# Performance work log

Measured on AMD Instinct MI355X. Metric: run time of the kernel, lower is better.

The kernel has to match this reference:

```python
import jax, jax.numpy as jnp
import numpy as np

N_NODES = 100000


def sage_layer(h, src, dst, w_self, w_neigh, b):
    """DGL SAGEConv with mean aggregator: fc_self(h) + fc_neigh(mean_in_neigh(h)) + b."""
    msg = h[src]  # [E, d] gather source features
    agg = jax.ops.segment_sum(msg, dst, num_segments=N_NODES)  # [N, d]
    deg = jax.ops.segment_sum(jnp.ones((src.shape[0],), h.dtype), dst, num_segments=N_NODES)
    mean = agg / jnp.maximum(deg, 1.0)[:, None]
    return h @ w_self + mean @ w_neigh + b


def setup_inputs() -> dict:
    key = jax.random.key(0)
    ks = jax.random.split(key, 12)
    N, E = N_NODES, 1600000
    in_f, hid, n_cls = 4, 128, 2

    def glorot(k, shape):
        lim = float(np.sqrt(6.0 / (shape[0] + shape[1])))
        return jax.random.uniform(k, shape, jnp.float32, -lim, lim)

    return {
        "feats": jax.random.normal(ks[0], (N, in_f), jnp.float32),
        "src": jax.random.randint(ks[1], (E,), 0, N),
        "dst": jax.random.randint(ks[2], (E,), 0, N),
        "w_self1": glorot(ks[3], (in_f, hid)),
        "w_neigh1": glorot(ks[4], (in_f, hid)),
        "b1": jnp.zeros((hid,), jnp.float32),
        "w_self2": glorot(ks[5], (hid, hid)),
        "w_neigh2": glorot(ks[6], (hid, hid)),
        "b2": jnp.zeros((hid,), jnp.float32),
        "w_out": glorot(ks[7], (hid, n_cls)),
        "b_out": jnp.zeros((n_cls,), jnp.float32),
    }


def reference(feats, src, dst, w_self1, w_neigh1, b1, w_self2, w_neigh2, b2, w_out, b_out):
    h = jax.nn.relu(sage_layer(feats, src, dst, w_self1, w_neigh1, b1))
    h = jax.nn.relu(sage_layer(h, src, dst, w_self2, w_neigh2, b2))
    return h @ w_out + b_out  # [N, num_classes] logits
```

## Files before the change

kernel.cpp:

```cpp
#include <hip/hip_runtime.h>
#include <hip/hip_bf16.h>

static constexpr int N = 100000;
static constexpr int HID = 128;
static constexpr int NBKT = (N + 127) / 128;
static constexpr int BCAP = 2560;
static constexpr int BEPB = 4096;

typedef short v8s __attribute__((ext_vector_type(8)));
typedef float v4f __attribute__((ext_vector_type(4)));
typedef unsigned short u16x8 __attribute__((ext_vector_type(8)));

static __device__ __forceinline__ unsigned short f2bf(float x) {
  unsigned u = __float_as_uint(x);
  return (unsigned short)((u + 0x7fffu + ((u >> 16) & 1u)) >> 16);
}
static __device__ __forceinline__ float bf2f(unsigned short u) {
  return __uint_as_float(((unsigned)u) << 16);
}

__global__ void k_wprep(const float* __restrict__ ws2, const float* __restrict__ wn2,
                        unsigned short* __restrict__ wp, unsigned* __restrict__ bcur) {
  int id = blockIdx.x * 64 + threadIdx.x;
  if (id < NBKT) bcur[id] = (unsigned)id * BCAP;
  int b = blockIdx.x;
  int mat = b >> 5;
  int ks = (b >> 3) & 3;
  int cf = b & 7;
  int l = threadIdx.x;
  const float* W = mat ? wn2 : ws2;
  int col = cf * 16 + (l & 15);
  int k0 = ks * 32 + (l >> 4) * 8;
  u16x8 h8, l8;
#pragma unroll
  for (int i = 0; i < 8; ++i) {
    float w = W[(k0 + i) * 128 + col];
    unsigned short h = f2bf(w);
    h8[i] = h;
    l8[i] = f2bf(w - bf2f(h));
  }
  int fhi = (ks * 4 + mat) * 8 + cf;
  int flo = (ks * 4 + mat + 2) * 8 + cf;
  *reinterpret_cast<u16x8*>(wp + fhi * 512 + l * 8) = h8;
  *reinterpret_cast<u16x8*>(wp + flo * 512 + l * 8) = l8;
}

__global__ __launch_bounds__(256) void k_bucket(const int* __restrict__ src,
                                                const int* __restrict__ dst,
                                                unsigned* __restrict__ bcur,
                                                unsigned* __restrict__ bucket, int E) {
  __shared__ unsigned hist[NBKT];
  __shared__ unsigned base[NBKT];
  for (int i = threadIdx.x; i < NBKT; i += 256) hist[i] = 0;
  __syncthreads();
  const int e0 = blockIdx.x * BEPB;
  const int n = min(e0 + BEPB, E) - e0;

  unsigned pk[16];
  int bk[16];
#pragma unroll
  for (int i = 0; i < 16; ++i) {
    int e = threadIdx.x + 256 * i;
    if (e < n) {
      int d = __builtin_nontemporal_load(dst + e0 + e);
      int s = __builtin_nontemporal_load(src + e0 + e);
      int b = d >> 7;
      pk[i] = ((unsigned)s << 7) | (unsigned)(d & 127);
      bk[i] = b;
      atomicAdd(&hist[b], 1u);
    } else {
      bk[i] = -1;
      pk[i] = 0;
    }
  }
  __syncthreads();
  for (int i = threadIdx.x; i < NBKT; i += 256) {
    unsigned h = hist[i];
    base[i] = h ? atomicAdd(&bcur[i], h) : 0u;
    hist[i] = 0;
  }
  __syncthreads();
#pragma unroll
  for (int i = 0; i < 16; ++i) {
    if (bk[i] >= 0) {
      unsigned pos = base[bk[i]] + atomicAdd(&hist[bk[i]], 1u);
      bucket[pos] = pk[i];
    }
  }
}

__global__ void k_bucketscan(const unsigned* __restrict__ bcur, unsigned* __restrict__ bbase) {
  __shared__ unsigned s[1024];
  int t = threadIdx.x;
  unsigned v = (t < NBKT) ? (bcur[t] - (unsigned)t * BCAP) : 0u;
  s[t] = v;
  __syncthreads();
  for (int off = 1; off < 1024; off <<= 1) {
    unsigned x = (t >= off) ? s[t - off] : 0u;
    __syncthreads();
    s[t] += x;
    __syncthreads();
  }
  if (t < NBKT) bbase[t] = s[t] - v;
}

__global__ __launch_bounds__(256) void k_csr(const unsigned* __restrict__ bcur,
                                             const unsigned* __restrict__ bbase,
                                             const unsigned* __restrict__ bucket,
                                             unsigned* __restrict__ cnt,
                                             unsigned* __restrict__ roff,
                                             int* __restrict__ csr) {
  const int b = blockIdx.x;
  const unsigned segbase = (unsigned)b * BCAP;
  const unsigned n = bcur[b] - segbase;
  const int v0 = b << 7;
  __shared__ unsigned h[128];
  __shared__ unsigned rowoff[128];
  __shared__ unsigned s[128];
  if (threadIdx.x < 128) h[threadIdx.x] = 0;
  __syncthreads();

  unsigned pk[10];
#pragma unroll
  for (int i = 0; i < 10; ++i) {
    unsigned idx = threadIdx.x + 256u * i;
    if (idx < n) {
      pk[i] = bucket[segbase + idx];
      atomicAdd(&h[pk[i] & 127u], 1u);
    } else {
      pk[i] = 0xffffffffu;
    }
  }
  __syncthreads();

  unsigned val = (threadIdx.x < 128) ? h[threadIdx.x] : 0u;
  if (threadIdx.x < 128) s[threadIdx.x] = val;
  __syncthreads();
  for (int off = 1; off < 128; off <<= 1) {
    unsigned x = (threadIdx.x < 128 && threadIdx.x >= off) ? s[threadIdx.x - off] : 0u;
    __syncthreads();
    if (threadIdx.x < 128) s[threadIdx.x] += x;
    __syncthreads();
  }
  if (threadIdx.x < 128) {
    int v = v0 + threadIdx.x;
    if (v < N) {
      unsigned rstart = bbase[b] + s[threadIdx.x] - val;
      rowoff[threadIdx.x] = rstart;
      roff[v] = rstart;
      cnt[v] = val;
    }
    h[threadIdx.x] = 0;
  }
  __syncthreads();

#pragma unroll
  for (int i = 0; i < 10; ++i) {
    if (pk[i] != 0xffffffffu) {
      unsigned dl = pk[i] & 127u;
      unsigned pos = rowoff[dl] + atomicAdd(&h[dl], 1u);
      csr[pos] = (int)(pk[i] >> 7);
    }
  }
}

__global__ void k_layer1(const float* __restrict__ feats, const unsigned* __restrict__ cnt,
                         const unsigned* __restrict__ roff, const int* __restrict__ csr,
                         const float* __restrict__ ws1, const float* __restrict__ wn1,
                         const float* __restrict__ b1, unsigned short* __restrict__ h1) {
  const int v = blockIdx.x * 16 + (threadIdx.x >> 4);
  const int l = threadIdx.x & 15;
  if (v >= N) return;
  const unsigned c = cnt[v];
  const unsigned start = roff[v];
  float4 acc = make_float4(0.f, 0.f, 0.f, 0.f);
  for (unsigned e = l; e < c; e += 16) {
    int s = csr[start + e];
    float4 f = *reinterpret_cast<const float4*>(feats + 4 * s);
    acc.x += f.x; acc.y += f.y; acc.z += f.z; acc.w += f.w;
  }
#pragma unroll
  for (int off = 1; off < 16; off <<= 1) {
    acc.x += __shfl_xor(acc.x, off);
    acc.y += __shfl_xor(acc.y, off);
    acc.z += __shfl_xor(acc.z, off);
    acc.w += __shfl_xor(acc.w, off);
  }
  float inv = 1.0f / fmaxf((float)c, 1.0f);
  float m0 = acc.x * inv, m1 = acc.y * inv, m2 = acc.z * inv, m3 = acc.w * inv;
  float4 fv = *reinterpret_cast<const float4*>(feats + 4 * v);
  const int c0 = l * 8;
  unsigned o[4];
#pragma unroll
  for (int half = 0; half < 2; ++half) {
    float4 bv = *reinterpret_cast<const float4*>(b1 + c0 + 4 * half);
    float ob[4] = {bv.x, bv.y, bv.z, bv.w};
#pragma unroll
    for (int k = 0; k < 4; ++k) {
      float4 wsv = *reinterpret_cast<const float4*>(ws1 + k * 128 + c0 + 4 * half);
      float4 wnv = *reinterpret_cast<const float4*>(wn1 + k * 128 + c0 + 4 * half);
      float fk = (k == 0) ? fv.x : (k == 1) ? fv.y : (k == 2) ? fv.z : fv.w;
      float mk = (k == 0) ? m0 : (k == 1) ? m1 : (k == 2) ? m2 : m3;
      ob[0] += fk * wsv.x + mk * wnv.x;
      ob[1] += fk * wsv.y + mk * wnv.y;
      ob[2] += fk * wsv.z + mk * wnv.z;
      ob[3] += fk * wsv.w + mk * wnv.w;
    }
#pragma unroll
    for (int jj = 0; jj < 2; ++jj) {
      float lo = fmaxf(ob[2 * jj], 0.f), hi = fmaxf(ob[2 * jj + 1], 0.f);
      o[2 * half + jj] = (unsigned)f2bf(lo) | (((unsigned)f2bf(hi)) << 16);
    }
  }
  *reinterpret_cast<uint4*>(h1 + (size_t)v * HID + c0) =
      make_uint4(o[0], o[1], o[2], o[3]);
}

__global__ void k_agg(const unsigned* __restrict__ cnt, const unsigned* __restrict__ roff,
                      const int* __restrict__ csr, const unsigned short* __restrict__ h1,
                      unsigned short* __restrict__ mean) {
  const int wv = threadIdx.x >> 6;
  const int lane = threadIdx.x & 63;
  const int hl = lane & 31;
  const int v = blockIdx.x * 8 + wv * 2 + (lane >> 5);
  if (v >= N) return;
  const unsigned c = cnt[v];
  const unsigned start = roff[v];
  const unsigned short* __restrict__ hrow = h1 + hl * 4;

  float a0 = 0.f, a1 = 0.f, a2 = 0.f, a3 = 0.f;
  float b0 = 0.f, b1 = 0.f, b2 = 0.f, b3 = 0.f;

  const unsigned cm = c & ~3u;
  unsigned e = 0;
  for (; e < cm; e += 4) {
    int s[4];
#pragma unroll
    for (int q = 0; q < 4; ++q) s[q] = csr[start + e + q];
    uint2 pk[4];
#pragma unroll
    for (int q = 0; q < 4; ++q)
      pk[q] = *reinterpret_cast<const uint2*>(hrow + (size_t)s[q] * HID);
#pragma unroll
    for (int q = 0; q < 4; ++q) {
      float f0 = __uint_as_float(pk[q].x << 16);
      float f1 = __uint_as_float(pk[q].x & 0xffff0000u);
      float f2 = __uint_as_float(pk[q].y << 16);
      float f3 = __uint_as_float(pk[q].y & 0xffff0000u);
      if (q & 1) { b0 += f0; b1 += f1; b2 += f2; b3 += f3; }
      else       { a0 += f0; a1 += f1; a2 += f2; a3 += f3; }
    }
  }
  for (; e < c; ++e) {
    int s = csr[start + e];
    uint2 pk = *reinterpret_cast<const uint2*>(hrow + (size_t)s * HID);
    a0 += __uint_as_float(pk.x << 16);
    a1 += __uint_as_float(pk.x & 0xffff0000u);
    a2 += __uint_as_float(pk.y << 16);
    a3 += __uint_as_float(pk.y & 0xffff0000u);
  }
  float inv = 1.0f / fmaxf((float)c, 1.0f);
  a0 = (a0 + b0) * inv; a1 = (a1 + b1) * inv;
  a2 = (a2 + b2) * inv; a3 = (a3 + b3) * inv;
  uint2 o;
  o.x = (unsigned)f2bf(a0) | (((unsigned)f2bf(a1)) << 16);
  o.y = (unsigned)f2bf(a2) | (((unsigned)f2bf(a3)) << 16);
  *reinterpret_cast<uint2*>(mean + (size_t)v * HID + hl * 4) = o;
}

__global__ __launch_bounds__(256) void k_l2_mfma(
    const unsigned short* __restrict__ h1, const unsigned short* __restrict__ mean,
    const unsigned short* __restrict__ wp, const float* __restrict__ b2,
    const float* __restrict__ wout, const float* __restrict__ bout,
    float* __restrict__ out) {
  const int l = threadIdx.x & 63;
  const int wv = threadIdx.x >> 6;
  const size_t vbase = (size_t)blockIdx.x * 64 + (size_t)wv * 16;
  const int rlane = l & 15;
  const int kg = l >> 4;

  size_t hr = vbase + rlane;
  if (hr >= N) hr = N - 1;
  v8s ah[4], am[4];
#pragma unroll
  for (int ks = 0; ks < 4; ++ks) {
    size_t off = hr * HID + ks * 32 + kg * 8;
    ah[ks] = *reinterpret_cast<const v8s*>(h1 + off);
    am[ks] = *reinterpret_cast<const v8s*>(mean + off);
  }

  v4f acc[8];
#pragma unroll
  for (int cf = 0; cf < 8; ++cf) acc[cf] = (v4f)(0.f);

#pragma unroll
  for (int ks = 0; ks < 4; ++ks) {
#pragma unroll
    for (int m = 0; m < 4; ++m) {
#pragma unroll
      for (int cf = 0; cf < 8; ++cf) {
        v8s bf = *reinterpret_cast<const v8s*>(wp + ((ks * 4 + m) * 8 + cf) * 512 + l * 8);
        acc[cf] = __builtin_amdgcn_mfma_f32_16x16x32_bf16(
            (m & 1) ? am[ks] : ah[ks], bf, acc[cf], 0, 0, 0);
      }
    }
  }

  float b2c[8], w0c[8], w1c[8];
#pragma unroll
  for (int cf = 0; cf < 8; ++cf) {
    int col = cf * 16 + rlane;
    b2c[cf] = b2[col];
    w0c[cf] = wout[col * 2 + 0];
    w1c[cf] = wout[col * 2 + 1];
  }
  const float bo0 = bout[0], bo1 = bout[1];
#pragma unroll
  for (int j = 0; j < 4; ++j) {
    float s0 = 0.f, s1 = 0.f;
#pragma unroll
    for (int cf = 0; cf < 8; ++cf) {
      float h2 = fmaxf(acc[cf][j] + b2c[cf], 0.f);
      s0 += h2 * w0c[cf];
      s1 += h2 * w1c[cf];
    }
#pragma unroll
    for (int off = 1; off < 16; off <<= 1) {
      s0 += __shfl_xor(s0, off);
      s1 += __shfl_xor(s1, off);
    }
    size_t row = vbase + kg * 4 + j;
    if (row < N) {
      if (rlane == 0) out[row * 2 + 0] = s0 + bo0;
      if (rlane == 1) out[row * 2 + 1] = s1 + bo1;
    }
  }
}

extern "C" void kernel_launch(void* const* d_in, const int* in_sizes, int n_in,
                              void* d_out, int out_size, void* d_ws, size_t ws_size,
                              hipStream_t stream) {
  const float* feats = (const float*)d_in[0];
  const int* src = (const int*)d_in[1];
  const int* dst = (const int*)d_in[2];
  const float* ws1 = (const float*)d_in[3];
  const float* wn1 = (const float*)d_in[4];
  const float* b1 = (const float*)d_in[5];
  const float* ws2 = (const float*)d_in[6];
  const float* wn2 = (const float*)d_in[7];
  const float* b2 = (const float*)d_in[8];
  const float* wout = (const float*)d_in[9];
  const float* bout = (const float*)d_in[10];
  float* out = (float*)d_out;
  const int E = in_sizes[1];

  char* p = (char*)d_ws;
  unsigned* bcur = (unsigned*)p;             p += 784 * 4;
  unsigned* bbase = (unsigned*)p;            p += 784 * 4;
  unsigned* bucket = (unsigned*)p;           p += (size_t)NBKT * BCAP * 4;
  int* csr = (int*)p;                        p += (size_t)E * 4;
  unsigned* cnt = (unsigned*)p;              p += (size_t)N * 4;
  unsigned* roff = (unsigned*)p;             p += (size_t)N * 4;
  unsigned short* h1 = (unsigned short*)p;   p += (size_t)N * HID * 2;
  unsigned short* mean = (unsigned short*)p; p += (size_t)N * HID * 2;
  unsigned short* wp = (unsigned short*)p;

  int bgrid = (E + BEPB - 1) / BEPB;
  k_wprep<<<64, 64, 0, stream>>>(ws2, wn2, wp, bcur);
  k_bucket<<<bgrid, 256, 0, stream>>>(src, dst, bcur, bucket, E);
  k_bucketscan<<<1, 1024, 0, stream>>>(bcur, bbase);
  k_csr<<<NBKT, 256, 0, stream>>>(bcur, bbase, bucket, cnt, roff, csr);
  k_layer1<<<(N + 15) / 16, 256, 0, stream>>>(feats, cnt, roff, csr, ws1, wn1, b1, h1);
  k_agg<<<(N + 7) / 8, 256, 0, stream>>>(cnt, roff, csr, h1, mean);
  k_l2_mfma<<<(N + 63) / 64, 256, 0, stream>>>(h1, mean, wp, b2, wout, bout, out);
}
```

Baseline: 168.6 us.

## Locally sort edges by bucket before scatter; double rows per wave in layer-2 MFMA

The bucketing kernel now stages each block's edges in shared memory and counting-sorts them by destination bucket with a block-wide prefix scan. The global writes then go out in bucket-contiguous runs, which makes them more coalesced than the previous random scatter. The layer-2 MFMA kernel now processes two 16-row fragments per wave, so each weight fragment loaded from memory feeds two MFMAs. The cost is a much larger shared-memory footprint and extra scan barriers in k_bucket, plus more registers and half as many blocks in k_l2_mfma.

```diff
diff --git a/kernel.cpp b/kernel.cpp
--- a/kernel.cpp
+++ b/kernel.cpp
@@ -49,43 +49,65 @@
                                                 const int* __restrict__ dst,
                                                 unsigned* __restrict__ bcur,
                                                 unsigned* __restrict__ bucket, int E) {
+  __shared__ unsigned pk_s[BEPB];
+  __shared__ unsigned short bk_s[BEPB];
+  __shared__ unsigned short rk_s[BEPB];
+  __shared__ unsigned sorted_pk[BEPB];
+  __shared__ unsigned short sorted_bk[BEPB];
   __shared__ unsigned hist[NBKT];
-  __shared__ unsigned base[NBKT];
-  for (int i = threadIdx.x; i < NBKT; i += 256) hist[i] = 0;
+  __shared__ unsigned lstart[NBKT];
+  __shared__ unsigned gadj[NBKT];
+  __shared__ unsigned s256[256];
+  __shared__ unsigned carry_s;
+  const int t = threadIdx.x;
+  for (int i = t; i < NBKT; i += 256) hist[i] = 0;
+  if (t == 0) carry_s = 0;
   __syncthreads();
   const int e0 = blockIdx.x * BEPB;
   const int n = min(e0 + BEPB, E) - e0;
 
-  unsigned pk[16];
-  int bk[16];
-#pragma unroll
-  for (int i = 0; i < 16; ++i) {
-    int e = threadIdx.x + 256 * i;
-    if (e < n) {
-      int d = __builtin_nontemporal_load(dst + e0 + e);
-      int s = __builtin_nontemporal_load(src + e0 + e);
-      int b = d >> 7;
-      pk[i] = ((unsigned)s << 7) | (unsigned)(d & 127);
-      bk[i] = b;
-      atomicAdd(&hist[b], 1u);
-    } else {
-      bk[i] = -1;
-      pk[i] = 0;
-    }
-  }
-  __syncthreads();
-  for (int i = threadIdx.x; i < NBKT; i += 256) {
-    unsigned h = hist[i];
-    base[i] = h ? atomicAdd(&bcur[i], h) : 0u;
-    hist[i] = 0;
-  }
-  __syncthreads();
-#pragma unroll
-  for (int i = 0; i < 16; ++i) {
-    if (bk[i] >= 0) {
-      unsigned pos = base[bk[i]] + atomicAdd(&hist[bk[i]], 1u);
-      bucket[pos] = pk[i];
-    }
+  for (int i = t; i < n; i += 256) {
+    int d = __builtin_nontemporal_load(dst + e0 + i);
+    int s = __builtin_nontemporal_load(src + e0 + i);
+    int p = d >> 7;
+    pk_s[i] = ((unsigned)s << 7) | (unsigned)(d & 127);
+    bk_s[i] = (unsigned short)p;
+    rk_s[i] = (unsigned short)atomicAdd(&hist[p], 1u);
+  }
+  __syncthreads();
+
+  for (int base = 0; base < NBKT; base += 256) {
+    int idx = base + t;
+    unsigned v = (idx < NBKT) ? hist[idx] : 0u;
+    s256[t] = v;
+    __syncthreads();
+    for (int off = 1; off < 256; off <<= 1) {
+      unsigned x = (t >= off) ? s256[t - off] : 0u;
+      __syncthreads();
+      s256[t] += x;
+      __syncthreads();
+    }
+    if (idx < NBKT) lstart[idx] = carry_s + s256[t] - v;
+    __syncthreads();
+    if (t == 255) carry_s += s256[255];
+    __syncthreads();
+  }
+
+  for (int i = t; i < NBKT; i += 256) {
+    unsigned c = hist[i];
+    gadj[i] = c ? (atomicAdd(&bcur[i], c) - lstart[i]) : 0u;
+  }
+  __syncthreads();
+
+  for (int i = t; i < n; i += 256) {
+    unsigned j = lstart[bk_s[i]] + (unsigned)rk_s[i];
+    sorted_pk[j] = pk_s[i];
+    sorted_bk[j] = bk_s[i];
+  }
+  __syncthreads();
+
+  for (int j = t; j < n; j += 256) {
+    bucket[gadj[sorted_bk[j]] + (unsigned)j] = sorted_pk[j];
   }
 }
 
@@ -275,23 +297,28 @@
     float* __restrict__ out) {
   const int l = threadIdx.x & 63;
   const int wv = threadIdx.x >> 6;
-  const size_t vbase = (size_t)blockIdx.x * 64 + (size_t)wv * 16;
+  const size_t vbase = (size_t)blockIdx.x * 128 + (size_t)wv * 32;
   const int rlane = l & 15;
   const int kg = l >> 4;
 
-  size_t hr = vbase + rlane;
-  if (hr >= N) hr = N - 1;
-  v8s ah[4], am[4];
-#pragma unroll
-  for (int ks = 0; ks < 4; ++ks) {
-    size_t off = hr * HID + ks * 32 + kg * 8;
-    ah[ks] = *reinterpret_cast<const v8s*>(h1 + off);
-    am[ks] = *reinterpret_cast<const v8s*>(mean + off);
-  }
-
-  v4f acc[8];
-#pragma unroll
-  for (int cf = 0; cf < 8; ++cf) acc[cf] = (v4f)(0.f);
+  v8s ah[2][4], am[2][4];
+#pragma unroll
+  for (int rf = 0; rf < 2; ++rf) {
+    size_t hr = vbase + rf * 16 + rlane;
+    if (hr >= N) hr = N - 1;
+#pragma unroll
+    for (int ks = 0; ks < 4; ++ks) {
+      size_t off = hr * HID + ks * 32 + kg * 8;
+      ah[rf][ks] = *reinterpret_cast<const v8s*>(h1 + off);
+      am[rf][ks] = *reinterpret_cast<const v8s*>(mean + off);
+    }
+  }
+
+  v4f acc[2][8];
+#pragma unroll
+  for (int rf = 0; rf < 2; ++rf)
+#pragma unroll
+    for (int cf = 0; cf < 8; ++cf) acc[rf][cf] = (v4f)(0.f);
 
 #pragma unroll
   for (int ks = 0; ks < 4; ++ks) {
@@ -300,8 +327,10 @@
 #pragma unroll
       for (int cf = 0; cf < 8; ++cf) {
         v8s bf = *reinterpret_cast<const v8s*>(wp + ((ks * 4 + m) * 8 + cf) * 512 + l * 8);
-        acc[cf] = __builtin_amdgcn_mfma_f32_16x16x32_bf16(
-            (m & 1) ? am[ks] : ah[ks], bf, acc[cf], 0, 0, 0);
+        acc[0][cf] = __builtin_amdgcn_mfma_f32_16x16x32_bf16(
+            (m & 1) ? am[0][ks] : ah[0][ks], bf, acc[0][cf], 0, 0, 0);
+        acc[1][cf] = __builtin_amdgcn_mfma_f32_16x16x32_bf16(
+            (m & 1) ? am[1][ks] : ah[1][ks], bf, acc[1][cf], 0, 0, 0);
       }
     }
   }
@@ -316,23 +345,26 @@
   }
   const float bo0 = bout[0], bo1 = bout[1];
 #pragma unroll
-  for (int j = 0; j < 4; ++j) {
-    float s0 = 0.f, s1 = 0.f;
-#pragma unroll
-    for (int cf = 0; cf < 8; ++cf) {
-      float h2 = fmaxf(acc[cf][j] + b2c[cf], 0.f);
-      s0 += h2 * w0c[cf];
-      s1 += h2 * w1c[cf];
-    }
-#pragma unroll
-    for (int off = 1; off < 16; off <<= 1) {
-      s0 += __shfl_xor(s0, off);
-      s1 += __shfl_xor(s1, off);
-    }
-    size_t row = vbase + kg * 4 + j;
-    if (row < N) {
-      if (rlane == 0) out[row * 2 + 0] = s0 + bo0;
-      if (rlane == 1) out[row * 2 + 1] = s1 + bo1;
+  for (int rf = 0; rf < 2; ++rf) {
+#pragma unroll
+    for (int j = 0; j < 4; ++j) {
+      float s0 = 0.f, s1 = 0.f;
+#pragma unroll
+      for (int cf = 0; cf < 8; ++cf) {
+        float h2 = fmaxf(acc[rf][cf][j] + b2c[cf], 0.f);
+        s0 += h2 * w0c[cf];
+        s1 += h2 * w1c[cf];
+      }
+#pragma unroll
+      for (int off = 1; off < 16; off <<= 1) {
+        s0 += __shfl_xor(s0, off);
+        s1 += __shfl_xor(s1, off);
+      }
+      size_t row = vbase + rf * 16 + kg * 4 + j;
+      if (row < N) {
+        if (rlane == 0) out[row * 2 + 0] = s0 + bo0;
+        if (rlane == 1) out[row * 2 + 1] = s1 + bo1;
+      }
     }
   }
 }
@@ -372,5 +404,5 @@
   k_csr<<<NBKT, 256, 0, stream>>>(bcur, bbase, bucket, cnt, roff, csr);
   k_layer1<<<(N + 15) / 16, 256, 0, stream>>>(feats, cnt, roff, csr, ws1, wn1, b1, h1);
   k_agg<<<(N + 7) / 8, 256, 0, stream>>>(cnt, roff, csr, h1, mean);
-  k_l2_mfma<<<(N + 63) / 64, 256, 0, stream>>>(h1, mean, wp, b2, wout, bout, out);
-}
+  k_l2_mfma<<<(N + 127) / 128, 256, 0, stream>>>(h1, mean, wp, b2, wout, bout, out);
+}
```

Result: slower. 176.1 us (+4.4%).

## Fuse layer-1 aggregation and linear into CSR build kernel via shared atomics

Applied to the files above, without the earlier changes.

The separate layer-1 kernel is removed. The CSR construction kernel now gathers source features while it reads each bucket, and accumulates per-destination sums in shared memory with float atomics. After the scan, each block computes the layer-1 linear, ReLU and bf16 output for its 128 nodes. This saves one kernel launch and a second pass over the CSR indices, at the cost of extra LDS atomic contention, a scattered gather inside k_csr, and summation order that is no longer deterministic.

```diff
diff --git a/kernel.cpp b/kernel.cpp
--- a/kernel.cpp
+++ b/kernel.cpp
@@ -104,12 +104,13 @@
   if (t < NBKT) bbase[t] = s[t] - v;
 }
 
-__global__ __launch_bounds__(256) void k_csr(const unsigned* __restrict__ bcur,
-                                             const unsigned* __restrict__ bbase,
-                                             const unsigned* __restrict__ bucket,
-                                             unsigned* __restrict__ cnt,
-                                             unsigned* __restrict__ roff,
-                                             int* __restrict__ csr) {
+__global__ __launch_bounds__(256) void k_csr(
+    const unsigned* __restrict__ bcur, const unsigned* __restrict__ bbase,
+    const unsigned* __restrict__ bucket, const float* __restrict__ feats,
+    const float* __restrict__ ws1, const float* __restrict__ wn1,
+    const float* __restrict__ b1, unsigned* __restrict__ cnt,
+    unsigned* __restrict__ roff, int* __restrict__ csr,
+    unsigned short* __restrict__ h1) {
   const int b = blockIdx.x;
   const unsigned segbase = (unsigned)b * BCAP;
   const unsigned n = bcur[b] - segbase;
@@ -117,40 +118,55 @@
   __shared__ unsigned h[128];
   __shared__ unsigned rowoff[128];
   __shared__ unsigned s[128];
-  if (threadIdx.x < 128) h[threadIdx.x] = 0;
+  __shared__ unsigned ccnt[128];
+  __shared__ float macc[128][4];
+  const int t = threadIdx.x;
+  if (t < 128) {
+    h[t] = 0;
+    macc[t][0] = 0.f; macc[t][1] = 0.f; macc[t][2] = 0.f; macc[t][3] = 0.f;
+  }
   __syncthreads();
 
   unsigned pk[10];
 #pragma unroll
   for (int i = 0; i < 10; ++i) {
-    unsigned idx = threadIdx.x + 256u * i;
-    if (idx < n) {
-      pk[i] = bucket[segbase + idx];
-      atomicAdd(&h[pk[i] & 127u], 1u);
-    } else {
-      pk[i] = 0xffffffffu;
-    }
-  }
-  __syncthreads();
-
-  unsigned val = (threadIdx.x < 128) ? h[threadIdx.x] : 0u;
-  if (threadIdx.x < 128) s[threadIdx.x] = val;
+    unsigned idx = t + 256u * i;
+    pk[i] = (idx < n) ? bucket[segbase + idx] : 0xffffffffu;
+  }
+#pragma unroll
+  for (int i = 0; i < 10; ++i) {
+    if (pk[i] != 0xffffffffu) {
+      unsigned dl = pk[i] & 127u;
+      int sv = (int)(pk[i] >> 7);
+      float4 f = *reinterpret_cast<const float4*>(feats + 4 * sv);
+      atomicAdd(&h[dl], 1u);
+      atomicAdd(&macc[dl][0], f.x);
+      atomicAdd(&macc[dl][1], f.y);
+      atomicAdd(&macc[dl][2], f.z);
+      atomicAdd(&macc[dl][3], f.w);
+    }
+  }
+  __syncthreads();
+
+  unsigned val = (t < 128) ? h[t] : 0u;
+  if (t < 128) s[t] = val;
   __syncthreads();
   for (int off = 1; off < 128; off <<= 1) {
-    unsigned x = (threadIdx.x < 128 && threadIdx.x >= off) ? s[threadIdx.x - off] : 0u;
+    unsigned x = (t < 128 && t >= off) ? s[t - off] : 0u;
     __syncthreads();
-    if (threadIdx.x < 128) s[threadIdx.x] += x;
+    if (t < 128) s[t] += x;
     __syncthreads();
   }
-  if (threadIdx.x < 128) {
-    int v = v0 + threadIdx.x;
+  if (t < 128) {
+    int v = v0 + t;
     if (v < N) {
-      unsigned rstart = bbase[b] + s[threadIdx.x] - val;
-      rowoff[threadIdx.x] = rstart;
+      unsigned rstart = bbase[b] + s[t] - val;
+      rowoff[t] = rstart;
       roff[v] = rstart;
       cnt[v] = val;
     }
-    h[threadIdx.x] = 0;
+    ccnt[t] = val;
+    h[t] = 0;
   }
   __syncthreads();
 
@@ -162,58 +178,44 @@
       csr[pos] = (int)(pk[i] >> 7);
     }
   }
-}
-
-__global__ void k_layer1(const float* __restrict__ feats, const unsigned* __restrict__ cnt,
-                         const unsigned* __restrict__ roff, const int* __restrict__ csr,
-                         const float* __restrict__ ws1, const float* __restrict__ wn1,
-                         const float* __restrict__ b1, unsigned short* __restrict__ h1) {
-  const int v = blockIdx.x * 16 + (threadIdx.x >> 4);
-  const int l = threadIdx.x & 15;
-  if (v >= N) return;
-  const unsigned c = cnt[v];
-  const unsigned start = roff[v];
-  float4 acc = make_float4(0.f, 0.f, 0.f, 0.f);
-  for (unsigned e = l; e < c; e += 16) {
-    int s = csr[start + e];
-    float4 f = *reinterpret_cast<const float4*>(feats + 4 * s);
-    acc.x += f.x; acc.y += f.y; acc.z += f.z; acc.w += f.w;
-  }
-#pragma unroll
-  for (int off = 1; off < 16; off <<= 1) {
-    acc.x += __shfl_xor(acc.x, off);
-    acc.y += __shfl_xor(acc.y, off);
-    acc.z += __shfl_xor(acc.z, off);
-    acc.w += __shfl_xor(acc.w, off);
-  }
-  float inv = 1.0f / fmaxf((float)c, 1.0f);
-  float m0 = acc.x * inv, m1 = acc.y * inv, m2 = acc.z * inv, m3 = acc.w * inv;
-  float4 fv = *reinterpret_cast<const float4*>(feats + 4 * v);
-  const int c0 = l * 8;
-  unsigned o[4];
-#pragma unroll
-  for (int half = 0; half < 2; ++half) {
-    float4 bv = *reinterpret_cast<const float4*>(b1 + c0 + 4 * half);
-    float ob[4] = {bv.x, bv.y, bv.z, bv.w};
-#pragma unroll
-    for (int k = 0; k < 4; ++k) {
-      float4 wsv = *reinterpret_cast<const float4*>(ws1 + k * 128 + c0 + 4 * half);
-      float4 wnv = *reinterpret_cast<const float4*>(wn1 + k * 128 + c0 + 4 * half);
-      float fk = (k == 0) ? fv.x : (k == 1) ? fv.y : (k == 2) ? fv.z : fv.w;
-      float mk = (k == 0) ? m0 : (k == 1) ? m1 : (k == 2) ? m2 : m3;
-      ob[0] += fk * wsv.x + mk * wnv.x;
-      ob[1] += fk * wsv.y + mk * wnv.y;
-      ob[2] += fk * wsv.z + mk * wnv.z;
-      ob[3] += fk * wsv.w + mk * wnv.w;
-    }
-#pragma unroll
-    for (int jj = 0; jj < 2; ++jj) {
-      float lo = fmaxf(ob[2 * jj], 0.f), hi = fmaxf(ob[2 * jj + 1], 0.f);
-      o[2 * half + jj] = (unsigned)f2bf(lo) | (((unsigned)f2bf(hi)) << 16);
-    }
-  }
-  *reinterpret_cast<uint4*>(h1 + (size_t)v * HID + c0) =
-      make_uint4(o[0], o[1], o[2], o[3]);
+
+  const int vl = t >> 1;
+  const int ch = (t & 1) * 64;
+  const int v = v0 + vl;
+  if (v < N) {
+    float inv = 1.0f / fmaxf((float)ccnt[vl], 1.0f);
+    float m0 = macc[vl][0] * inv, m1 = macc[vl][1] * inv;
+    float m2 = macc[vl][2] * inv, m3 = macc[vl][3] * inv;
+    float4 fv = *reinterpret_cast<const float4*>(feats + 4 * v);
+#pragma unroll
+    for (int g = 0; g < 8; ++g) {
+      const int c0 = ch + 8 * g;
+      unsigned o[4];
+#pragma unroll
+      for (int half = 0; half < 2; ++half) {
+        float4 bv = *reinterpret_cast<const float4*>(b1 + c0 + 4 * half);
+        float ob[4] = {bv.x, bv.y, bv.z, bv.w};
+#pragma unroll
+        for (int k = 0; k < 4; ++k) {
+          float4 wsv = *reinterpret_cast<const float4*>(ws1 + k * 128 + c0 + 4 * half);
+          float4 wnv = *reinterpret_cast<const float4*>(wn1 + k * 128 + c0 + 4 * half);
+          float fk = (k == 0) ? fv.x : (k == 1) ? fv.y : (k == 2) ? fv.z : fv.w;
+          float mk = (k == 0) ? m0 : (k == 1) ? m1 : (k == 2) ? m2 : m3;
+          ob[0] += fk * wsv.x + mk * wnv.x;
+          ob[1] += fk * wsv.y + mk * wnv.y;
+          ob[2] += fk * wsv.z + mk * wnv.z;
+          ob[3] += fk * wsv.w + mk * wnv.w;
+        }
+#pragma unroll
+        for (int jj = 0; jj < 2; ++jj) {
+          float lo = fmaxf(ob[2 * jj], 0.f), hi = fmaxf(ob[2 * jj + 1], 0.f);
+          o[2 * half + jj] = (unsigned)f2bf(lo) | (((unsigned)f2bf(hi)) << 16);
+        }
+      }
+      *reinterpret_cast<uint4*>(h1 + (size_t)v * HID + c0) =
+          make_uint4(o[0], o[1], o[2], o[3]);
+    }
+  }
 }
 
 __global__ void k_agg(const unsigned* __restrict__ cnt, const unsigned* __restrict__ roff,
@@ -369,8 +371,8 @@
   k_wprep<<<64, 64, 0, stream>>>(ws2, wn2, wp, bcur);
   k_bucket<<<bgrid, 256, 0, stream>>>(src, dst, bcur, bucket, E);
   k_bucketscan<<<1, 1024, 0, stream>>>(bcur, bbase);
-  k_csr<<<NBKT, 256, 0, stream>>>(bcur, bbase, bucket, cnt, roff, csr);
-  k_layer1<<<(N + 15) / 16, 256, 0, stream>>>(feats, cnt, roff, csr, ws1, wn1, b1, h1);
+  k_csr<<<NBKT, 256, 0, stream>>>(bcur, bbase, bucket, feats, ws1, wn1, b1,
+                                  cnt, roff, csr, h1);
   k_agg<<<(N + 7) / 8, 256, 0, stream>>>(cnt, roff, csr, h1, mean);
   k_l2_mfma<<<(N + 63) / 64, 256, 0, stream>>>(h1, mean, wp, b2, wout, bout, out);
 }
```

Result: slower. 219.5 us (+30.1%).
